# Kernel optimization log

Hardware: AMD Instinct MI355X
Metric: run time of the kernel (lower is better)

## Reference

```python
import jax, jax.numpy as jnp
import numpy as np

N_SITES = 100000
DIM = 128
KSIZE = 7  # 7^3 = 343 offsets
GRID = 160


def _build_sparse_structure(seed=0):
    """Sample N_SITES unique voxels in a GRID^3 volume and build the
    depthwise-conv kernel map: neighbor_idx[i, k] = index of site at
    coords[i] + offset[k], or N_SITES (sentinel -> zero row) if absent."""
    rng = np.random.default_rng(seed)
    lin = rng.choice(GRID ** 3, size=N_SITES, replace=False)
    coords = np.stack(np.unravel_index(lin, (GRID, GRID, GRID)), axis=1).astype(np.int64)  # [N,3]
    lookup = np.full(GRID ** 3, N_SITES, dtype=np.int32)
    lookup[lin] = np.arange(N_SITES, dtype=np.int32)
    r = KSIZE // 2
    offs = np.stack(np.meshgrid(*([np.arange(-r, r + 1)] * 3), indexing="ij"), axis=-1).reshape(-1, 3)  # [343,3]
    K = offs.shape[0]
    neighbor_idx = np.full((N_SITES, K), N_SITES, dtype=np.int32)
    for k in range(K):
        nb = coords + offs[k]
        ok = np.all((nb >= 0) & (nb < GRID), axis=1)
        nb_lin = (nb[ok, 0] * GRID + nb[ok, 1]) * GRID + nb[ok, 2]
        neighbor_idx[ok, k] = lookup[nb_lin]
    return neighbor_idx


def setup_inputs() -> dict:
    key = jax.random.key(0)
    ks = jax.random.split(key, 12)
    neighbor_idx = jnp.asarray(_build_sparse_structure(0))
    d, h = DIM, 4 * DIM
    K = KSIZE ** 3
    return {
        "feats": jax.random.normal(ks[0], (N_SITES, d), jnp.float32),
        "neighbor_idx": neighbor_idx,
        "dw_w": jax.random.normal(ks[1], (K, d), jnp.float32) * 0.05,
        "dw_b": jax.random.normal(ks[2], (d,), jnp.float32) * 0.02,
        "ln_g": 1.0 + 0.1 * jax.random.normal(ks[3], (d,), jnp.float32),
        "ln_b": 0.02 * jax.random.normal(ks[4], (d,), jnp.float32),
        "w1": jax.random.normal(ks[5], (d, h), jnp.float32) * (1.0 / np.sqrt(d)),
        "b1": 0.02 * jax.random.normal(ks[6], (h,), jnp.float32),
        "grn_g": 0.1 * jax.random.normal(ks[7], (1, h), jnp.float32),
        "grn_b": 0.02 * jax.random.normal(ks[8], (1, h), jnp.float32),
        "w2": jax.random.normal(ks[9], (h, d), jnp.float32) * (1.0 / np.sqrt(h)),
        "b2": 0.02 * jax.random.normal(ks[10], (d,), jnp.float32),
    }


def reference(feats, neighbor_idx, dw_w, dw_b, ln_g, ln_b, w1, b1, grn_g, grn_b, w2, b2):
    eps = 1e-6
    n, d = feats.shape
    # --- sparse depthwise conv: gather-multiply-accumulate over kernel offsets ---
    f_pad = jnp.concatenate([feats, jnp.zeros((1, d), feats.dtype)], axis=0)  # sentinel row

    def step(acc, xs):
        idx_k, w_k = xs  # idx_k: [N], w_k: [dim]
        return acc + f_pad[idx_k] * w_k, None

    x, _ = jax.lax.scan(step, jnp.zeros_like(feats), (neighbor_idx.T, dw_w))
    x = x + dw_b
    # --- LayerNorm over channels ---
    mu = jnp.mean(x, axis=-1, keepdims=True)
    var = jnp.var(x, axis=-1, keepdims=True)
    x = (x - mu) / jnp.sqrt(var + eps) * ln_g + ln_b
    # --- pwconv1 -> GELU (exact, matching torch default) ---
    x = jax.nn.gelu(x @ w1 + b1, approximate=False)  # [N, 4*dim]
    # --- GRN: L2 norm over all sites (dim=0), per channel ---
    gx = jnp.sqrt(jnp.sum(x * x, axis=0, keepdims=True))  # [1, 4*dim]
    nx = gx / (jnp.mean(gx, axis=-1, keepdims=True) + eps)
    x = grn_g * (x * nx) + grn_b + x
    # --- pwconv2 + residual (drop_path identity in eval) ---
    x = x @ w2 + b2
    return feats + x
```

## Files before the change

### kernel.cpp

```cpp
#include <hip/hip_runtime.h>

typedef unsigned short u16;
typedef unsigned int u32;
typedef __attribute__((ext_vector_type(8))) short bf16x8;
typedef __attribute__((ext_vector_type(4))) float f32x4;

__device__ __forceinline__ u16 f2bf(float f) {
    u32 u = __float_as_uint(f);
    return (u16)((u + 0x7FFFu + ((u >> 16) & 1u)) >> 16);
}

__device__ __forceinline__ float fast_gelu(float x) {
    const float t = x * x;
    const float y2 = x * __builtin_fmaf(0.0713548214f, t, 1.5957691216057308f);
    const float u = __expf(fminf(y2, 80.f));
    return x * u * __builtin_amdgcn_rcpf(u + 1.f);
}

__device__ __forceinline__ void gload_lds16(const u16* g, u16* l) {
    __builtin_amdgcn_global_load_lds(
        (const __attribute__((address_space(1))) void*)g,
        (__attribute__((address_space(3))) void*)l, 16, 0, 0);
}

__global__ __launch_bounds__(256) void cast_feats_k(
    const float* __restrict__ src, u16* __restrict__ dst, int n4)
{
    const int e = blockIdx.x * 256 + threadIdx.x;
    if (e >= n4) return;
    const float4 v = *(const float4*)(src + (size_t)e * 4);
    uint2 o;
    o.x = (u32)f2bf(v.x) | ((u32)f2bf(v.y) << 16);
    o.y = (u32)f2bf(v.z) | ((u32)f2bf(v.w) << 16);
    *(uint2*)(dst + (size_t)e * 4) = o;
}

__global__ __launch_bounds__(256) void dwln_k(
    const u16* __restrict__ featsb, const int* __restrict__ nb,
    const u16* __restrict__ dwwb, const float* __restrict__ dw_b,
    const float* __restrict__ ln_g, const float* __restrict__ ln_b,
    u16* __restrict__ xln, int nsites)
{
    __shared__ int lists[4][352];
    const int w = threadIdx.x >> 6;
    const int lane = threadIdx.x & 63;
    const int s = blockIdx.x * 4 + w;
    if (s >= nsites) return;
    const int* row = nb + (size_t)s * 343;
    int idx[6];
    #pragma unroll
    for (int j = 0; j < 5; ++j) idx[j] = row[lane + j * 64];
    idx[5] = (lane < 23) ? row[320 + lane] : nsites;
    const unsigned long long below = ((1ull << lane) - 1ull);
    int cnt = 0;
    #pragma unroll
    for (int i = 0; i < 6; ++i) {
        const bool v = idx[i] < nsites;
        const unsigned long long bal = __ballot(v);
        const int k = (i < 5) ? (lane + i * 64) : (320 + lane);
        if (v) lists[w][cnt + __popcll(bal & below)] = idx[i] | (k << 17);
        cnt += (int)__popcll(bal);
    }
    const int cntp = (cnt + 7) & ~7;
    if (lane < cntp - cnt) lists[w][cnt + lane] = nsites;
    __builtin_amdgcn_s_waitcnt(0);
    float x0 = 0.f, x1 = 0.f;
    for (int base = 0; base < cntp; base += 8) {
        u32 f[8], wv[8];
        #pragma unroll
        for (int i = 0; i < 8; ++i) {
            const int e = lists[w][base + i];
            f[i]  = *(const u32*)(featsb + (size_t)(e & 0x1FFFF) * 128 + lane * 2);
            wv[i] = *(const u32*)(dwwb + (size_t)(e >> 17) * 128 + lane * 2);
        }
        #pragma unroll
        for (int i = 0; i < 8; ++i) {
            x0 += __uint_as_float(f[i] << 16) * __uint_as_float(wv[i] << 16);
            x1 += __uint_as_float(f[i] & 0xFFFF0000u) * __uint_as_float(wv[i] & 0xFFFF0000u);
        }
    }
    const float2 bv = *(const float2*)(dw_b + lane * 2);
    const float2 gv = *(const float2*)(ln_g + lane * 2);
    const float2 lbv = *(const float2*)(ln_b + lane * 2);
    float a0 = x0 + bv.x, a1 = x1 + bv.y;
    float sm = a0 + a1, ss = a0 * a0 + a1 * a1;
    #pragma unroll
    for (int off = 32; off > 0; off >>= 1) {
        sm += __shfl_xor(sm, off, 64);
        ss += __shfl_xor(ss, off, 64);
    }
    const float mean = sm * (1.f / 128.f);
    const float var = ss * (1.f / 128.f) - mean * mean;
    const float rstd = rsqrtf(fmaxf(var, 0.f) + 1e-6f);
    const float y0 = (a0 - mean) * rstd * gv.x + lbv.x;
    const float y1 = (a1 - mean) * rstd * gv.y + lbv.y;
    *(u32*)(xln + (size_t)s * 128 + lane * 2) =
        (u32)f2bf(y0) | ((u32)f2bf(y1) << 16);
}

__global__ __launch_bounds__(256) void transpose_w1_k(
    const float* __restrict__ w1, u16* __restrict__ w1t)
{
    const int e = blockIdx.x * 256 + threadIdx.x;
    const int n = e >> 7, k = e & 127;
    w1t[e] = f2bf(w1[k * 512 + n]);
}

__global__ __launch_bounds__(256, 4) void gemm1_k(
    const u16* __restrict__ xln, const u16* __restrict__ w1t,
    const float* __restrict__ b1, u16* __restrict__ h,
    float* __restrict__ gx_sq, int nsites)
{
    __shared__ u16 xb[64 * 128];
    __shared__ float s_red[128];
    const int t = threadIdx.x;
    const int n0 = blockIdx.x * 128;
    const int m0 = blockIdx.y * 64;
    const int lane = t & 63;
    const int w = t >> 6;
    const int wn = w * 32;
    const int l15 = lane & 15, quad = lane >> 4;
    if (t < 128) s_red[t] = 0.f;
    #pragma unroll
    for (int i = 0; i < 4; ++i) {
        const int r = w * 16 + i * 4 + (lane >> 4);
        const int c = (lane & 15) ^ (r & 15);
        gload_lds16(xln + (size_t)(m0 + r) * 128 + c * 8,
                    &xb[(w * 16 + i * 4) * 128]);
    }
    f32x4 acc[2][4];
    #pragma unroll
    for (int i = 0; i < 2; ++i)
        #pragma unroll
        for (int j = 0; j < 4; ++j) acc[i][j] = f32x4{0.f, 0.f, 0.f, 0.f};
    const u16* a_base = w1t + (size_t)(n0 + wn + l15) * 128 + quad * 8;
    bf16x8 aC[2];
    #pragma unroll
    for (int nt = 0; nt < 2; ++nt) aC[nt] = *(const bf16x8*)(a_base + (size_t)nt * 16 * 128);
    asm volatile("s_waitcnt vmcnt(0)" ::: "memory");
    __syncthreads();
    #pragma unroll
    for (int ks = 0; ks < 4; ++ks) {
        bf16x8 aN[2];
        if (ks < 3) {
            #pragma unroll
            for (int nt = 0; nt < 2; ++nt)
                aN[nt] = *(const bf16x8*)(a_base + (size_t)nt * 16 * 128 + (ks + 1) * 32);
        }
        bf16x8 b[4];
        #pragma unroll
        for (int mt = 0; mt < 4; ++mt) {
            const int r = mt * 16 + l15;
            b[mt] = *(const bf16x8*)(&xb[r * 128 + (((ks * 4 + quad) ^ l15) << 3)]);
        }
        #pragma unroll
        for (int nt = 0; nt < 2; ++nt)
            #pragma unroll
            for (int mt = 0; mt < 4; ++mt)
                acc[nt][mt] = __builtin_amdgcn_mfma_f32_16x16x32_bf16(aC[nt], b[mt], acc[nt][mt], 0, 0, 0);
        if (ks < 3) {
            #pragma unroll
            for (int nt = 0; nt < 2; ++nt) aC[nt] = aN[nt];
        }
    }
    float ssl[2][4] = {{0.f,0.f,0.f,0.f},{0.f,0.f,0.f,0.f}};
    #pragma unroll
    for (int nt = 0; nt < 2; ++nt) {
        const int chb = n0 + wn + nt * 16 + quad * 4;
        const float4 b1v = *(const float4*)(b1 + chb);
        #pragma unroll
        for (int mt = 0; mt < 4; ++mt) {
            const int site = m0 + mt * 16 + l15;
            if (site < nsites) {
                float v[4];
                #pragma unroll
                for (int rg = 0; rg < 4; ++rg) {
                    v[rg] = fast_gelu(acc[nt][mt][rg] + ((const float*)&b1v)[rg]);
                    ssl[nt][rg] += v[rg] * v[rg];
                }
                uint2 o;
                o.x = (u32)f2bf(v[0]) | ((u32)f2bf(v[1]) << 16);
                o.y = (u32)f2bf(v[2]) | ((u32)f2bf(v[3]) << 16);
                *(uint2*)(h + (size_t)site * 512 + chb) = o;
            }
        }
    }
    #pragma unroll
    for (int nt = 0; nt < 2; ++nt)
        #pragma unroll
        for (int rg = 0; rg < 4; ++rg) {
            float v = ssl[nt][rg];
            v += __shfl_xor(v, 1, 64);
            v += __shfl_xor(v, 2, 64);
            v += __shfl_xor(v, 4, 64);
            v += __shfl_xor(v, 8, 64);
            if (l15 == 0) atomicAdd(&s_red[wn + nt * 16 + quad * 4 + rg], v);
        }
    __syncthreads();
    if (t < 128) atomicAdd(&gx_sq[n0 + t], s_red[t]);
}

__global__ __launch_bounds__(256) void beff_k(
    const float* __restrict__ grn_b, const float* __restrict__ w2,
    float* __restrict__ b_eff)
{
    __shared__ float red[256];
    const int t = threadIdx.x;
    const int dc = t & 127, part = t >> 7;
    const int c0 = blockIdx.x * 64 + part * 32;
    float p = 0.f;
    #pragma unroll 8
    for (int i = 0; i < 32; ++i) {
        const int c = c0 + i;
        p += grn_b[c] * w2[(size_t)c * 128 + dc];
    }
    red[t] = p;
    __syncthreads();
    if (t < 128) atomicAdd(&b_eff[t], red[t] + red[t + 128]);
}

__global__ __launch_bounds__(512) void grn_scale_k(
    const float* __restrict__ gx_sq, const float* __restrict__ grn_g,
    float* __restrict__ scale)
{
    __shared__ float red[512];
    const int t = threadIdx.x;
    const float g = sqrtf(gx_sq[t]);
    red[t] = g;
    __syncthreads();
    #pragma unroll
    for (int off = 256; off > 0; off >>= 1) {
        if (t < off) red[t] += red[t + off];
        __syncthreads();
    }
    const float mean = red[0] * (1.f / 512.f);
    scale[t] = grn_g[t] * (g / (mean + 1e-6f)) + 1.f;
}

__global__ __launch_bounds__(256) void w2t_k(
    const float* __restrict__ scale, const float* __restrict__ w2,
    u16* __restrict__ w2t)
{
    const int e = blockIdx.x * 256 + threadIdx.x;
    const int c = e & 511, dc = e >> 9;
    w2t[e] = f2bf(scale[c] * w2[(size_t)c * 128 + dc]);
}

__global__ __launch_bounds__(256, 4) void gemm2_k(
    const u16* __restrict__ h, const u16* __restrict__ w2t,
    const float* __restrict__ b_eff, const float* __restrict__ b2,
    const float* __restrict__ feats,
    float* __restrict__ out, int nsites)
{
    __shared__ u16 hb[2][64 * 128];
    const int t = threadIdx.x;
    const int m0 = blockIdx.x * 64;
    const int lane = t & 63;
    const int w = t >> 6;
    const int wn = w * 32;
    const int l15 = lane & 15, quad = lane >> 4;
    f32x4 acc[2][4];
    #pragma unroll
    for (int i = 0; i < 2; ++i)
        #pragma unroll
        for (int j = 0; j < 4; ++j) acc[i][j] = f32x4{0.f, 0.f, 0.f, 0.f};
    const u16* a_base = w2t + (size_t)(wn + l15) * 512 + quad * 8;

    #define STAGE2(bsel, tc)                                                     \
        {                                                                        \
            _Pragma("unroll")                                                    \
            for (int i_ = 0; i_ < 4; ++i_) {                                     \
                const int r_ = w * 16 + i_ * 4 + (lane >> 4);                    \
                const int c_ = (lane & 15) ^ (r_ & 15);                          \
                gload_lds16(h + (size_t)(m0 + r_) * 512 + (tc) * 128 + c_ * 8,   \
                            &hb[bsel][(w * 16 + i_ * 4) * 128]);                 \
            }                                                                    \
        }

    STAGE2(0, 0)
    bf16x8 aC[2];
    #pragma unroll
    for (int nt = 0; nt < 2; ++nt) aC[nt] = *(const bf16x8*)(a_base + (size_t)nt * 16 * 512);
    asm volatile("s_waitcnt vmcnt(0)" ::: "memory");
    __syncthreads();
    #pragma unroll
    for (int tch = 0; tch < 4; ++tch) {
        const int cur = tch & 1;
        if (tch < 3) STAGE2(cur ^ 1, tch + 1)
        #pragma unroll
        for (int ks = 0; ks < 4; ++ks) {
            const int ksg = tch * 4 + ks;
            bf16x8 aN[2];
            if (ksg < 15) {
                #pragma unroll
                for (int nt = 0; nt < 2; ++nt)
                    aN[nt] = *(const bf16x8*)(a_base + (size_t)nt * 16 * 512 + (ksg + 1) * 32);
            }
            bf16x8 b[4];
            #pragma unroll
            for (int mt = 0; mt < 4; ++mt) {
                const int r = mt * 16 + l15;
                b[mt] = *(const bf16x8*)(&hb[cur][r * 128 + (((ks * 4 + quad) ^ l15) << 3)]);
            }
            #pragma unroll
            for (int nt = 0; nt < 2; ++nt)
                #pragma unroll
                for (int mt = 0; mt < 4; ++mt)
                    acc[nt][mt] = __builtin_amdgcn_mfma_f32_16x16x32_bf16(aC[nt], b[mt], acc[nt][mt], 0, 0, 0);
            if (ksg < 15) {
                #pragma unroll
                for (int nt = 0; nt < 2; ++nt) aC[nt] = aN[nt];
            }
        }
        if (tch < 3) {
            asm volatile("s_waitcnt vmcnt(0)" ::: "memory");
            __syncthreads();
        }
    }
    #undef STAGE2
    #pragma unroll
    for (int nt = 0; nt < 2; ++nt) {
        const int chb = wn + nt * 16 + quad * 4;
        const float4 bev = *(const float4*)(b_eff + chb);
        const float4 b2v = *(const float4*)(b2 + chb);
        #pragma unroll
        for (int mt = 0; mt < 4; ++mt) {
            const int site = m0 + mt * 16 + l15;
            if (site < nsites) {
                const float4 fv = *(const float4*)(feats + (size_t)site * 128 + chb);
                float4 o;
                o.x = acc[nt][mt][0] + bev.x + b2v.x + fv.x;
                o.y = acc[nt][mt][1] + bev.y + b2v.y + fv.y;
                o.z = acc[nt][mt][2] + bev.z + b2v.z + fv.z;
                o.w = acc[nt][mt][3] + bev.w + b2v.w + fv.w;
                *(float4*)(out + (size_t)site * 128 + chb) = o;
            }
        }
    }
}

extern "C" void kernel_launch(void* const* d_in, const int* in_sizes, int n_in,
                              void* d_out, int out_size, void* d_ws, size_t ws_size,
                              hipStream_t stream) {
    const float* feats = (const float*)d_in[0];
    const int* nb      = (const int*)d_in[1];
    const float* dw_w  = (const float*)d_in[2];
    const float* dw_b  = (const float*)d_in[3];
    const float* ln_g  = (const float*)d_in[4];
    const float* ln_b  = (const float*)d_in[5];
    const float* w1    = (const float*)d_in[6];
    const float* b1    = (const float*)d_in[7];
    const float* grn_g = (const float*)d_in[8];
    const float* grn_b = (const float*)d_in[9];
    const float* w2    = (const float*)d_in[10];
    const float* b2    = (const float*)d_in[11];
    float* out = (float*)d_out;
    const int nsites = in_sizes[0] / 128;

    char* ws = (char*)d_ws;
    size_t off = 0;
    u16* xln   = (u16*)(ws + off);  off += (((size_t)(nsites + 128) * 128 * 2) + 255) & ~(size_t)255;
    u16* h     = (u16*)(ws + off);  off += (((size_t)(nsites + 128) * 512 * 2) + 255) & ~(size_t)255;
    u16* featsb= (u16*)(ws + off);  off += (((size_t)(nsites + 1) * 128 * 2) + 255) & ~(size_t)255;
    u16* dwwb  = (u16*)(ws + off);  off += 343 * 128 * 2 + 128;
    u16* w1t   = (u16*)(ws + off);  off += 512 * 128 * 2;
    u16* w2t   = (u16*)(ws + off);  off += 128 * 512 * 2;
    float* gx_sq = (float*)(ws + off); off += 512 * 4;
    float* scale = (float*)(ws + off); off += 512 * 4;
    float* b_eff = (float*)(ws + off); off += 128 * 4;

    hipMemsetAsync(gx_sq, 0, 512 * sizeof(float), stream);
    hipMemsetAsync(b_eff, 0, 128 * sizeof(float), stream);
    hipMemsetAsync(featsb + (size_t)nsites * 128, 0, 128 * sizeof(u16), stream);
    const int nfeat4 = nsites * 32;
    cast_feats_k<<<(nfeat4 + 255) / 256, 256, 0, stream>>>(feats, featsb, nfeat4);
    const int ndww4 = 343 * 32;
    cast_feats_k<<<(ndww4 + 255) / 256, 256, 0, stream>>>(dw_w, dwwb, ndww4);
    transpose_w1_k<<<256, 256, 0, stream>>>(w1, w1t);
    beff_k<<<8, 256, 0, stream>>>(grn_b, w2, b_eff);
    dwln_k<<<(nsites + 3) / 4, 256, 0, stream>>>(featsb, nb, dwwb, dw_b, ln_g, ln_b, xln, nsites);
    const int m1blocks = (nsites + 63) / 64;
    gemm1_k<<<dim3(4, m1blocks), 256, 0, stream>>>(xln, w1t, b1, h, gx_sq, nsites);
    grn_scale_k<<<1, 512, 0, stream>>>(gx_sq, grn_g, scale);
    w2t_k<<<256, 256, 0, stream>>>(scale, w2, w2t);
    const int m2blocks = (nsites + 63) / 64;
    gemm2_k<<<m2blocks, 256, 0, stream>>>(h, w2t, b_eff, b2, feats, out, nsites);
}
```

Before: 413.0 us.

## Make gemm1 persistent with double-buffered LDS prefetch and register-resident weights

Turns gemm1 into a persistent kernel: the grid is capped at 4x256 blocks, and each block loops over 64-row M tiles with a stride of gridDim.y. The next tile's activations are loaded into a second LDS buffer while the current tile is computed. The block's full W1 fragment is kept in registers across tiles, and the per-channel sum of squares is reduced once per block rather than once per tile. This removes per-tile launch and prologue overhead and the many global atomics, in exchange for double the LDS, higher register pressure, and fewer blocks in flight.

```diff
diff --git a/kernel.cpp b/kernel.cpp
--- a/kernel.cpp
+++ b/kernel.cpp
@@ -109,82 +109,93 @@
 __global__ __launch_bounds__(256, 4) void gemm1_k(
     const u16* __restrict__ xln, const u16* __restrict__ w1t,
     const float* __restrict__ b1, u16* __restrict__ h,
-    float* __restrict__ gx_sq, int nsites)
-{
-    __shared__ u16 xb[64 * 128];
+    float* __restrict__ gx_sq, int nsites, int nmb)
+{
+    __shared__ u16 xb[2][64 * 128];
     __shared__ float s_red[128];
     const int t = threadIdx.x;
     const int n0 = blockIdx.x * 128;
-    const int m0 = blockIdx.y * 64;
     const int lane = t & 63;
     const int w = t >> 6;
     const int wn = w * 32;
     const int l15 = lane & 15, quad = lane >> 4;
     if (t < 128) s_red[t] = 0.f;
-    #pragma unroll
-    for (int i = 0; i < 4; ++i) {
-        const int r = w * 16 + i * 4 + (lane >> 4);
-        const int c = (lane & 15) ^ (r & 15);
-        gload_lds16(xln + (size_t)(m0 + r) * 128 + c * 8,
-                    &xb[(w * 16 + i * 4) * 128]);
-    }
-    f32x4 acc[2][4];
-    #pragma unroll
-    for (int i = 0; i < 2; ++i)
-        #pragma unroll
-        for (int j = 0; j < 4; ++j) acc[i][j] = f32x4{0.f, 0.f, 0.f, 0.f};
+
+    #define STAGE1(bsel, mb_)                                                    \
+        {                                                                        \
+            _Pragma("unroll")                                                    \
+            for (int i_ = 0; i_ < 4; ++i_) {                                     \
+                const int r_ = w * 16 + i_ * 4 + (lane >> 4);                    \
+                const int c_ = (lane & 15) ^ (r_ & 15);                          \
+                gload_lds16(xln + (size_t)((mb_) * 64 + r_) * 128 + c_ * 8,      \
+                            &xb[bsel][(w * 16 + i_ * 4) * 128]);                 \
+            }                                                                    \
+        }
+
+    int mb = blockIdx.y;
+    STAGE1(0, mb)
+    __builtin_amdgcn_sched_barrier(0);
     const u16* a_base = w1t + (size_t)(n0 + wn + l15) * 128 + quad * 8;
-    bf16x8 aC[2];
-    #pragma unroll
-    for (int nt = 0; nt < 2; ++nt) aC[nt] = *(const bf16x8*)(a_base + (size_t)nt * 16 * 128);
-    asm volatile("s_waitcnt vmcnt(0)" ::: "memory");
-    __syncthreads();
-    #pragma unroll
-    for (int ks = 0; ks < 4; ++ks) {
-        bf16x8 aN[2];
-        if (ks < 3) {
+    bf16x8 aF[4][2];
+    #pragma unroll
+    for (int ks = 0; ks < 4; ++ks)
+        #pragma unroll
+        for (int nt = 0; nt < 2; ++nt)
+            aF[ks][nt] = *(const bf16x8*)(a_base + (size_t)nt * 16 * 128 + ks * 32);
+
+    float ssl[2][4] = {{0.f,0.f,0.f,0.f},{0.f,0.f,0.f,0.f}};
+    int cur = 0;
+    while (mb < nmb) {
+        asm volatile("s_waitcnt vmcnt(8)" ::: "memory");
+        __builtin_amdgcn_s_barrier();
+        __builtin_amdgcn_sched_barrier(0);
+        const int mbn = mb + (int)gridDim.y;
+        if (mbn < nmb) STAGE1(cur ^ 1, mbn)
+        __builtin_amdgcn_sched_barrier(0);
+        const int m0 = mb * 64;
+        f32x4 acc[2][4];
+        #pragma unroll
+        for (int i = 0; i < 2; ++i)
+            #pragma unroll
+            for (int j = 0; j < 4; ++j) acc[i][j] = f32x4{0.f, 0.f, 0.f, 0.f};
+        #pragma unroll
+        for (int ks = 0; ks < 4; ++ks) {
+            bf16x8 b[4];
+            #pragma unroll
+            for (int mt = 0; mt < 4; ++mt) {
+                const int r = mt * 16 + l15;
+                b[mt] = *(const bf16x8*)(&xb[cur][r * 128 + (((ks * 4 + quad) ^ l15) << 3)]);
+            }
             #pragma unroll
             for (int nt = 0; nt < 2; ++nt)
-                aN[nt] = *(const bf16x8*)(a_base + (size_t)nt * 16 * 128 + (ks + 1) * 32);
-        }
-        bf16x8 b[4];
-        #pragma unroll
-        for (int mt = 0; mt < 4; ++mt) {
-            const int r = mt * 16 + l15;
-            b[mt] = *(const bf16x8*)(&xb[r * 128 + (((ks * 4 + quad) ^ l15) << 3)]);
-        }
-        #pragma unroll
-        for (int nt = 0; nt < 2; ++nt)
-            #pragma unroll
-            for (int mt = 0; mt < 4; ++mt)
-                acc[nt][mt] = __builtin_amdgcn_mfma_f32_16x16x32_bf16(aC[nt], b[mt], acc[nt][mt], 0, 0, 0);
-        if (ks < 3) {
-            #pragma unroll
-            for (int nt = 0; nt < 2; ++nt) aC[nt] = aN[nt];
-        }
-    }
-    float ssl[2][4] = {{0.f,0.f,0.f,0.f},{0.f,0.f,0.f,0.f}};
-    #pragma unroll
-    for (int nt = 0; nt < 2; ++nt) {
-        const int chb = n0 + wn + nt * 16 + quad * 4;
-        const float4 b1v = *(const float4*)(b1 + chb);
-        #pragma unroll
-        for (int mt = 0; mt < 4; ++mt) {
-            const int site = m0 + mt * 16 + l15;
-            if (site < nsites) {
-                float v[4];
                 #pragma unroll
-                for (int rg = 0; rg < 4; ++rg) {
-                    v[rg] = fast_gelu(acc[nt][mt][rg] + ((const float*)&b1v)[rg]);
-                    ssl[nt][rg] += v[rg] * v[rg];
+                for (int mt = 0; mt < 4; ++mt)
+                    acc[nt][mt] = __builtin_amdgcn_mfma_f32_16x16x32_bf16(aF[ks][nt], b[mt], acc[nt][mt], 0, 0, 0);
+        }
+        #pragma unroll
+        for (int nt = 0; nt < 2; ++nt) {
+            const int chb = n0 + wn + nt * 16 + quad * 4;
+            const float4 b1v = *(const float4*)(b1 + chb);
+            #pragma unroll
+            for (int mt = 0; mt < 4; ++mt) {
+                const int site = m0 + mt * 16 + l15;
+                if (site < nsites) {
+                    float v[4];
+                    #pragma unroll
+                    for (int rg = 0; rg < 4; ++rg) {
+                        v[rg] = fast_gelu(acc[nt][mt][rg] + ((const float*)&b1v)[rg]);
+                        ssl[nt][rg] += v[rg] * v[rg];
+                    }
+                    uint2 o;
+                    o.x = (u32)f2bf(v[0]) | ((u32)f2bf(v[1]) << 16);
+                    o.y = (u32)f2bf(v[2]) | ((u32)f2bf(v[3]) << 16);
+                    *(uint2*)(h + (size_t)site * 512 + chb) = o;
                 }
-                uint2 o;
-                o.x = (u32)f2bf(v[0]) | ((u32)f2bf(v[1]) << 16);
-                o.y = (u32)f2bf(v[2]) | ((u32)f2bf(v[3]) << 16);
-                *(uint2*)(h + (size_t)site * 512 + chb) = o;
-            }
-        }
-    }
+            }
+        }
+        mb = mbn; cur ^= 1;
+    }
+    #undef STAGE1
     #pragma unroll
     for (int nt = 0; nt < 2; ++nt)
         #pragma unroll
@@ -379,8 +390,9 @@
     transpose_w1_k<<<256, 256, 0, stream>>>(w1, w1t);
     beff_k<<<8, 256, 0, stream>>>(grn_b, w2, b_eff);
     dwln_k<<<(nsites + 3) / 4, 256, 0, stream>>>(featsb, nb, dwwb, dw_b, ln_g, ln_b, xln, nsites);
-    const int m1blocks = (nsites + 63) / 64;
-    gemm1_k<<<dim3(4, m1blocks), 256, 0, stream>>>(xln, w1t, b1, h, gx_sq, nsites);
+    const int nmb = (nsites + 63) / 64;
+    const int gy = nmb < 256 ? nmb : 256;
+    gemm1_k<<<dim3(4, gy), 256, 0, stream>>>(xln, w1t, b1, h, gx_sq, nsites, nmb);
     grn_scale_k<<<1, 512, 0, stream>>>(gx_sq, grn_g, scale);
     w2t_k<<<256, 256, 0, stream>>>(scale, w2, w2t);
     const int m2blocks = (nsites + 63) / 64;
```

Measured after the change: 404.1 us. 2.2% less time.
